# Kernel optimization log

Hardware: AMD Instinct MI355X
Metric: run time of the kernel (lower is better)

Reference implementation:

```python
import jax, jax.numpy as jnp
import numpy as np

B, N, L, D = 16, 8192, 512, 384  # batch, points, latents, model dim
FF = 4 * D  # feedforward inner dim (after GEGLU split)


def _ln(x, g, b, eps=1e-5):
    m = jnp.mean(x, axis=-1, keepdims=True)
    v = jnp.mean((x - m) ** 2, axis=-1, keepdims=True)
    return (x - m) * jax.lax.rsqrt(v + eps) * g + b


def setup_inputs() -> dict:
    key = jax.random.key(0)
    ks = jax.random.split(key, 16)
    s = 0.02
    def w(k, shape):
        return jax.random.normal(k, shape, jnp.float32) * s
    return {
        "x": jax.random.normal(ks[0], (B, N, 3), jnp.float32),
        # MLP: in(3)->D, D->D, D->D, D->D with ReLU between (eqx-style depth=3)
        "mlp_w0": w(ks[1], (3, D)), "mlp_b0": jnp.zeros((D,), jnp.float32),
        "mlp_w1": w(ks[2], (D, D)), "mlp_b1": jnp.zeros((D,), jnp.float32),
        "mlp_w2": w(ks[3], (D, D)), "mlp_b2": jnp.zeros((D,), jnp.float32),
        "mlp_w3": w(ks[4], (D, D)), "mlp_b3": jnp.zeros((D,), jnp.float32),
        "query": jax.random.normal(ks[5], (1, L, D), jnp.float32),
        "ln_q_g": jnp.ones((D,), jnp.float32), "ln_q_b": jnp.zeros((D,), jnp.float32),
        "ln_ctx_g": jnp.ones((D,), jnp.float32), "ln_ctx_b": jnp.zeros((D,), jnp.float32),
        "wq": w(ks[6], (D, D)),
        "wkv": w(ks[7], (D, 2 * D)),
        "wo": w(ks[8], (D, D)), "bo": jnp.zeros((D,), jnp.float32),
        "ln_ff_g": jnp.ones((D,), jnp.float32), "ln_ff_b": jnp.zeros((D,), jnp.float32),
        "ff_w1": w(ks[9], (D, 2 * FF)), "ff_b1": jnp.zeros((2 * FF,), jnp.float32),
        "ff_w2": w(ks[10], (FF, D)), "ff_b2": jnp.zeros((D,), jnp.float32),
    }


def reference(x, mlp_w0, mlp_b0, mlp_w1, mlp_b1, mlp_w2, mlp_b2, mlp_w3, mlp_b3,
              query, ln_q_g, ln_q_b, ln_ctx_g, ln_ctx_b, wq, wkv, wo, bo,
              ln_ff_g, ln_ff_b, ff_w1, ff_b1, ff_w2, ff_b2):
    # point MLP: 3 -> D
    h = jax.nn.relu(x @ mlp_w0 + mlp_b0)
    h = jax.nn.relu(h @ mlp_w1 + mlp_b1)
    h = jax.nn.relu(h @ mlp_w2 + mlp_b2)
    ctx = h @ mlp_w3 + mlp_b3                      # [B, N, D]

    lq = jnp.broadcast_to(query, (x.shape[0], L, D))  # learnable latents

    # PreNorm cross-attention (heads=1, dim_head=D)
    qn = _ln(lq, ln_q_g, ln_q_b)
    cn = _ln(ctx, ln_ctx_g, ln_ctx_b)
    q = qn @ wq                                    # [B, L, D]
    kv = cn @ wkv
    k, v = jnp.split(kv, 2, axis=-1)               # [B, N, D] each
    scale = D ** -0.5
    sim = jnp.einsum('bid,bjd->bij', q, k) * scale # [B, L, N]
    attn = jax.nn.softmax(sim, axis=-1)
    out = jnp.einsum('bij,bjd->bid', attn, v)      # [B, L, D]
    x1 = (out @ wo + bo) + lq                      # residual

    # PreNorm GEGLU feedforward
    f = _ln(x1, ln_ff_g, ln_ff_b)
    f = f @ ff_w1 + ff_b1                          # [B, L, 2*FF]
    a, g = jnp.split(f, 2, axis=-1)
    f = a * jax.nn.gelu(g, approximate=False)      # GEGLU (exact gelu, torch default)
    return (f @ ff_w2 + ff_b2) + x1                # [B, L, D]
```

## Files before the change

### kernel.cpp

```cpp
#include <hip/hip_runtime.h>
#include <math.h>


typedef unsigned short u16;
typedef unsigned int   u32;
typedef __bf16 bf16_t;
typedef bf16_t bf16x8 __attribute__((ext_vector_type(8)));
typedef float  floatx4 __attribute__((ext_vector_type(4)));

__device__ __forceinline__ float b2f(u16 v) {
    return __uint_as_float(((u32)v) << 16);
}
__device__ __forceinline__ u16 f2b(float f) {
    u32 u = __float_as_uint(f);
    return (u16)((u + 0x7FFFu + ((u >> 16) & 1u)) >> 16);
}
__device__ __forceinline__ void stb4(u16* p, float4 f) {
    uint2 v;
    v.x = (u32)f2b(f.x) | ((u32)f2b(f.y) << 16);
    v.y = (u32)f2b(f.z) | ((u32)f2b(f.w) << 16);
    *(uint2*)p = v;
}

__device__ __forceinline__ void gl2lds16(u16* lds, const u16* g) {
    __builtin_amdgcn_global_load_lds(
        (const __attribute__((address_space(1))) void*)g,
        (__attribute__((address_space(3))) void*)lds, 16, 0, 0);
}

__device__ __forceinline__ void xcd_remap(int& bx, int& by, int& bz) {
    int gx = gridDim.x, gy = gridDim.y, gz = gridDim.z;
    int nb = gx * gy * gz;
    int p = bx + gx * (by + gy * bz);
    if ((nb & 7) == 0) {
        int chunk = nb >> 3;
        p = (p & 7) * chunk + (p >> 3);
    }
    bx = p % gx;
    int t = p / gx;
    by = t % gy;
    bz = t / gy;
}

__device__ __forceinline__ void xcd_remap_yf(int& bx, int& by, int& bz) {
    int gx = gridDim.x, gy = gridDim.y, gz = gridDim.z;
    int nb = gx * gy * gz;
    int p = by + gy * (bx + gx * bz);
    if ((nb & 7) == 0) {
        int chunk = nb >> 3;
        p = (p & 7) * chunk + (p >> 3);
    }
    by = p % gy;
    int t = p / gy;
    bx = t % gx;
    bz = t / gx;
}

__global__ __launch_bounds__(256) void wconv_kernel(
    const float* __restrict__ W, u16* __restrict__ WT, int Kd, int Nd)
{
    int idx = blockIdx.x * 256 + threadIdx.x;
    if (idx >= Kd * Nd) return;
    int n = idx / Kd, k = idx - n * Kd;
    WT[idx] = f2b(W[(long long)k * Nd + n]);
}

__global__ __launch_bounds__(256) void layer0_kernel(
    const float* __restrict__ X, const float* __restrict__ W0,
    const float* __restrict__ B0, u16* __restrict__ H, int total4)
{
    int idx = blockIdx.x * 256 + threadIdx.x;
    if (idx >= total4) return;
    int e = idx * 4;
    int m = e / 384;
    int j = e - m * 384;
    float x0 = X[m * 3 + 0], x1 = X[m * 3 + 1], x2 = X[m * 3 + 2];
    float4 w0 = *(const float4*)(W0 + j);
    float4 w1 = *(const float4*)(W0 + 384 + j);
    float4 w2 = *(const float4*)(W0 + 768 + j);
    float4 bb = *(const float4*)(B0 + j);
    float4 v;
    v.x = fmaxf(bb.x + x0 * w0.x + x1 * w1.x + x2 * w2.x, 0.f);
    v.y = fmaxf(bb.y + x0 * w0.y + x1 * w1.y + x2 * w2.y, 0.f);
    v.z = fmaxf(bb.z + x0 * w0.z + x1 * w1.z + x2 * w2.z, 0.f);
    v.w = fmaxf(bb.w + x0 * w0.w + x1 * w1.w + x2 * w2.w, 0.f);
    stb4(H + e, v);
}

template<int IN_F32>
__global__ __launch_bounds__(256) void ln_kernel(
    const void* __restrict__ Xv, const float* __restrict__ g,
    const float* __restrict__ b, u16* __restrict__ Y, int rows)
{
    int w = threadIdx.x >> 6, lane = threadIdx.x & 63;
    int row = blockIdx.x * 4 + w;
    if (row >= rows) return;
    float v[6];
    float s = 0.f, ss = 0.f;
#pragma unroll
    for (int i = 0; i < 6; ++i) {
        int c = i * 64 + lane;
        v[i] = IN_F32 ? ((const float*)Xv)[(long long)row * 384 + c]
                      : b2f(((const u16*)Xv)[(long long)row * 384 + c]);
        s += v[i]; ss += v[i] * v[i];
    }
#pragma unroll
    for (int m = 32; m; m >>= 1) {
        s  += __shfl_xor(s, m, 64);
        ss += __shfl_xor(ss, m, 64);
    }
    float mean = s * (1.0f / 384.0f);
    float var  = ss * (1.0f / 384.0f) - mean * mean;
    float rs = rsqrtf(fmaxf(var, 0.f) + 1e-5f);
    u16* yr = Y + (long long)row * 384;
#pragma unroll
    for (int i = 0; i < 6; ++i) {
        int c = i * 64 + lane;
        yr[c] = f2b((v[i] - mean) * rs * g[c] + b[c]);
    }
}

#define STAGE_AB(bufi, kk)                                                     \
    { u16* asd_ = shmem + (bufi) * 4096;                                       \
      u16* bsd_ = shmem + 8192 + (bufi) * 4096;                                \
      gl2lds16(asd_ + (wv * 32) * 32,                                          \
          aptr_ + (long long)(m0 + wv * 32 + rlo_) * lda_ + (kk) + c8_);       \
      gl2lds16(asd_ + (wv * 32 + 16) * 32,                                     \
          aptr_ + (long long)(m0 + wv * 32 + 16 + rlo_) * lda_ + (kk) + c8_);  \
      gl2lds16(bsd_ + (wv * 32) * 32,                                          \
          bptr_ + (long long)(n0 + wv * 32 + rlo_) * ldb_ + (kk) + c8_);       \
      gl2lds16(bsd_ + (wv * 32 + 16) * 32,                                     \
          bptr_ + (long long)(n0 + wv * 32 + 16 + rlo_) * ldb_ + (kk) + c8_); }

#define MFMA_TILE_DBUF(Aptr, Bptr, LDA, LDB, K0, K1)                           \
    {                                                                          \
        const u16* aptr_ = (Aptr); const u16* bptr_ = (Bptr);                  \
        const long long lda_ = (LDA), ldb_ = (LDB);                            \
        const int rlo_ = lane >> 2, c8_ = (lane & 3) * 8;                      \
        int cur = 0;                                                           \
        STAGE_AB(0, (K0))                                                      \
        for (int k0 = (K0); k0 < (K1); k0 += 32) {                             \
            __syncthreads();           \
            if (k0 + 32 < (K1)) STAGE_AB(cur ^ 1, k0 + 32)                     \
            const u16* As_ = shmem + cur * 4096;                               \
            const u16* Bs_ = shmem + 8192 + cur * 4096;                        \
            bf16x8 a0 = *(const bf16x8*)&As_[(wv * 32 + lr) * 32 + lq * 8];    \
            bf16x8 a1 = *(const bf16x8*)&As_[(wv * 32 + 16 + lr) * 32 + lq * 8]; \
            _Pragma("unroll")                                                  \
            for (int ns = 0; ns < 8; ++ns) {                                   \
                bf16x8 b = *(const bf16x8*)&Bs_[(ns * 16 + lr) * 32 + lq * 8]; \
                acc[0][ns] = __builtin_amdgcn_mfma_f32_16x16x32_bf16(a0, b, acc[0][ns], 0, 0, 0); \
                acc[1][ns] = __builtin_amdgcn_mfma_f32_16x16x32_bf16(a1, b, acc[1][ns], 0, 0, 0); \
            }                                                                  \
            cur ^= 1;                                                          \
        }                                                                      \
    }

template<int RES_F32, int OUT_F32>
__global__ __launch_bounds__(256) void gemm_mfma(
    const u16* __restrict__ A, const u16* __restrict__ WT,
    const float* __restrict__ bias, const void* __restrict__ res,
    void* __restrict__ C,
    int M, int N, int K, int lda, int ldb, int ldc, int ldres,
    float scale, int relu, int resmask,
    long long zsA, long long zsB, long long zsC)
{
    __shared__ u16 shmem[16384];
    const int tid = threadIdx.x;
    const int wv = tid >> 6, lane = tid & 63;
    const int lr = lane & 15, lq = lane >> 4;
    int bx = blockIdx.x, by = blockIdx.y, bz = blockIdx.z;
    xcd_remap_yf(bx, by, bz);
    const int m0 = bx * 128;
    const int n0 = by * 128;
    const u16* Az = A + bz * zsA;
    const u16* Bz = WT + bz * zsB;
    const long long czoff = bz * zsC;

    floatx4 acc[2][8];
#pragma unroll
    for (int i = 0; i < 2; ++i)
#pragma unroll
        for (int j = 0; j < 8; ++j)
            acc[i][j] = (floatx4){0.f, 0.f, 0.f, 0.f};

    MFMA_TILE_DBUF(Az, Bz, lda, ldb, 0, K)

    float bi[8];
#pragma unroll
    for (int ns = 0; ns < 8; ++ns)
        bi[ns] = bias ? bias[n0 + ns * 16 + lr] : 0.f;

#pragma unroll
    for (int ms = 0; ms < 2; ++ms) {
#pragma unroll
        for (int r = 0; r < 4; ++r) {
            int m = m0 + wv * 32 + ms * 16 + lq * 4 + r;
#pragma unroll
            for (int ns = 0; ns < 8; ++ns) {
                int col = n0 + ns * 16 + lr;
                float v = acc[ms][ns][r] * scale + bi[ns];
                if (relu) v = fmaxf(v, 0.f);
                if (res) {
                    long long ro = (long long)(m & resmask) * ldres + col;
                    v += RES_F32 ? ((const float*)res)[ro]
                                 : b2f(((const u16*)res)[ro]);
                }
                long long co = czoff + (long long)m * ldc + col;
                if (OUT_F32) ((float*)C)[co] = v;
                else         ((u16*)C)[co] = f2b(v);
            }
        }
    }
}

__global__ __launch_bounds__(256) void gemm_exp(
    const u16* __restrict__ A, const u16* __restrict__ WT,
    u16* __restrict__ P, float* __restrict__ den,
    int K, int lda, int ldb, int ldc, float scale,
    long long zsB, long long zsP)
{
    __shared__ u16 shmem[16384];
    const int tid = threadIdx.x;
    const int wv = tid >> 6, lane = tid & 63;
    const int lr = lane & 15, lq = lane >> 4;
    int bx = blockIdx.x, by = blockIdx.y, bz = blockIdx.z;
    xcd_remap(bx, by, bz);
    const int m0 = bx * 128;
    const int n0 = by * 128;
    const u16* Bz = WT + bz * zsB;
    u16* Pz = P + bz * zsP;
    float* dz = den + bz * 512;

    floatx4 acc[2][8];
#pragma unroll
    for (int i = 0; i < 2; ++i)
#pragma unroll
        for (int j = 0; j < 8; ++j)
            acc[i][j] = (floatx4){0.f, 0.f, 0.f, 0.f};

    MFMA_TILE_DBUF(A, Bz, lda, ldb, 0, K)

    u16* sh = shmem;
    float srow[2][4] = {};
#pragma unroll
    for (int ms = 0; ms < 2; ++ms) {
        __syncthreads();
#pragma unroll
        for (int ns = 0; ns < 8; ++ns)
#pragma unroll
            for (int r = 0; r < 4; ++r) {
                float l = acc[ms][ns][r] * scale;
                l = fminf(fmaxf(l, -60.f), 60.f);
                float p = __expf(l);
                srow[ms][r] += p;
                sh[(wv * 16 + lq * 4 + r) * 128 + ns * 16 + lr] = f2b(p);
            }
        __syncthreads();
#pragma unroll
        for (int j = 0; j < 4; ++j) {
            int idx = j * 256 + tid;
            int rl = idx >> 4, ch = idx & 15;
            int m = m0 + ((rl >> 4) << 5) + ms * 16 + (rl & 15);
            *(uint4*)&Pz[(long long)m * ldc + n0 + ch * 8] =
                *(const uint4*)&sh[rl * 128 + ch * 8];
        }
    }
#pragma unroll
    for (int ms = 0; ms < 2; ++ms)
#pragma unroll
        for (int r = 0; r < 4; ++r) {
            float s = srow[ms][r];
            s += __shfl_xor(s, 1, 64);
            s += __shfl_xor(s, 2, 64);
            s += __shfl_xor(s, 4, 64);
            s += __shfl_xor(s, 8, 64);
            if (lr == 0)
                atomicAdd(&dz[m0 + wv * 32 + ms * 16 + lq * 4 + r], s);
        }
}

__global__ __launch_bounds__(256) void gemm_pv(
    const u16* __restrict__ P, const u16* __restrict__ VT,
    const float* __restrict__ den, u16* __restrict__ part, int SPLIT)
{
    __shared__ u16 shmem[16384];
    const int tid = threadIdx.x;
    const int wv = tid >> 6, lane = tid & 63;
    const int lr = lane & 15, lq = lane >> 4;
    int bx = blockIdx.x, by = blockIdx.y, bz = blockIdx.z;
    xcd_remap(bx, by, bz);
    const int m0 = bx * 128;
    const int n0 = by * 128;
    const int g = bz / SPLIT, sp = bz - g * SPLIT;
    const int chunk = 8192 / SPLIT;
    const u16* Az = P + (long long)g * 512 * 8192;
    const u16* Bz = VT + (long long)g * 384 * 8192;
    const float* dg = den + g * 512;

    floatx4 acc[2][8];
#pragma unroll
    for (int i = 0; i < 2; ++i)
#pragma unroll
        for (int j = 0; j < 8; ++j)
            acc[i][j] = (floatx4){0.f, 0.f, 0.f, 0.f};

    MFMA_TILE_DBUF(Az, Bz, 8192, 8192, sp * chunk, sp * chunk + chunk)

    u16* pz = part + (long long)bz * 512 * 384;
#pragma unroll
    for (int ms = 0; ms < 2; ++ms)
#pragma unroll
        for (int r = 0; r < 4; ++r) {
            int m = m0 + wv * 32 + ms * 16 + lq * 4 + r;
            float inv = 1.0f / dg[m];
#pragma unroll
            for (int ns = 0; ns < 8; ++ns) {
                int col = n0 + ns * 16 + lr;
                pz[(long long)m * 384 + col] = f2b(acc[ms][ns][r] * inv);
            }
        }
}

__global__ __launch_bounds__(256) void pv_reduce_kernel(
    const u16* __restrict__ part, u16* __restrict__ AO, int SPLIT)
{
    int idx = blockIdx.x * 256 + threadIdx.x;
    int q = idx / 96, j = (idx - q * 96) * 4;
    int g = q >> 9, ql = q & 511;
    const u16* base = part + ((long long)g * SPLIT * 512 + ql) * 384 + j;
    float4 s = make_float4(0.f, 0.f, 0.f, 0.f);
    for (int sp = 0; sp < SPLIT; ++sp) {
        uint2 v = *(const uint2*)(base + (long long)sp * 512 * 384);
        s.x += b2f((u16)(v.x & 0xffff));
        s.y += b2f((u16)(v.x >> 16));
        s.z += b2f((u16)(v.y & 0xffff));
        s.w += b2f((u16)(v.y >> 16));
    }
    stb4(AO + (long long)q * 384 + j, s);
}

__global__ __launch_bounds__(256) void gemm_ff1_geglu(
    const u16* __restrict__ A, const u16* __restrict__ WT,
    const float* __restrict__ bias, u16* __restrict__ C,
    int K, int lda, int ldb, int ldc)
{
    __shared__ u16 shmem[16384];
    const int tid = threadIdx.x;
    const int wv = tid >> 6, lane = tid & 63;
    const int lr = lane & 15, lq = lane >> 4;
    int bx = blockIdx.x, by = blockIdx.y, bz = blockIdx.z;
    xcd_remap_yf(bx, by, bz);
    const int m0 = bx * 128;
    const int n0 = by * 64;
    const int rlo = lane >> 2, c8 = (lane & 3) * 8;

    floatx4 accA[2][4], accG[2][4];
#pragma unroll
    for (int i = 0; i < 2; ++i)
#pragma unroll
        for (int j = 0; j < 4; ++j) {
            accA[i][j] = (floatx4){0.f, 0.f, 0.f, 0.f};
            accG[i][j] = (floatx4){0.f, 0.f, 0.f, 0.f};
        }

#define STAGE_FF(bufi, kk)                                                     \
    { u16* asd = shmem + (bufi) * 4096;                                        \
      u16* bsd = shmem + 8192 + (bufi) * 4096;                                 \
      gl2lds16(asd + (wv * 32) * 32,                                           \
          A + (long long)(m0 + wv * 32 + rlo) * lda + (kk) + c8);              \
      gl2lds16(asd + (wv * 32 + 16) * 32,                                      \
          A + (long long)(m0 + wv * 32 + 16 + rlo) * lda + (kk) + c8);         \
      int r0 = wv * 32 + rlo, r1 = r0 + 16;                                    \
      int wrow0 = (r0 < 64) ? (n0 + r0) : (1536 + n0 + r0 - 64);               \
      int wrow1 = (r1 < 64) ? (n0 + r1) : (1536 + n0 + r1 - 64);               \
      gl2lds16(bsd + (wv * 32) * 32, WT + (long long)wrow0 * ldb + (kk) + c8); \
      gl2lds16(bsd + (wv * 32 + 16) * 32, WT + (long long)wrow1 * ldb + (kk) + c8); }

    int cur = 0;
    STAGE_FF(0, 0)
    for (int k0 = 0; k0 < K; k0 += 32) {
        __syncthreads();
        if (k0 + 32 < K) STAGE_FF(cur ^ 1, k0 + 32)
        const u16* As_ = shmem + cur * 4096;
        const u16* Bs_ = shmem + 8192 + cur * 4096;
        bf16x8 a0 = *(const bf16x8*)&As_[(wv * 32 + lr) * 32 + lq * 8];
        bf16x8 a1 = *(const bf16x8*)&As_[(wv * 32 + 16 + lr) * 32 + lq * 8];
#pragma unroll
        for (int ns = 0; ns < 4; ++ns) {
            bf16x8 bA = *(const bf16x8*)&Bs_[(ns * 16 + lr) * 32 + lq * 8];
            bf16x8 bG = *(const bf16x8*)&Bs_[((64 + ns * 16) + lr) * 32 + lq * 8];
            accA[0][ns] = __builtin_amdgcn_mfma_f32_16x16x32_bf16(a0, bA, accA[0][ns], 0, 0, 0);
            accA[1][ns] = __builtin_amdgcn_mfma_f32_16x16x32_bf16(a1, bA, accA[1][ns], 0, 0, 0);
            accG[0][ns] = __builtin_amdgcn_mfma_f32_16x16x32_bf16(a0, bG, accG[0][ns], 0, 0, 0);
            accG[1][ns] = __builtin_amdgcn_mfma_f32_16x16x32_bf16(a1, bG, accG[1][ns], 0, 0, 0);
        }
        cur ^= 1;
    }
#undef STAGE_FF

    float ba[4], bg[4];
#pragma unroll
    for (int ns = 0; ns < 4; ++ns) {
        ba[ns] = bias[n0 + ns * 16 + lr];
        bg[ns] = bias[1536 + n0 + ns * 16 + lr];
    }
#pragma unroll
    for (int ms = 0; ms < 2; ++ms)
#pragma unroll
        for (int r = 0; r < 4; ++r) {
            int m = m0 + wv * 32 + ms * 16 + lq * 4 + r;
#pragma unroll
            for (int ns = 0; ns < 4; ++ns) {
                int col = n0 + ns * 16 + lr;
                float a = accA[ms][ns][r] + ba[ns];
                float g = accG[ms][ns][r] + bg[ns];
                float v = a * 0.5f * g * (1.0f + erff(g * 0.70710678118654752f));
                C[(long long)m * ldc + col] = f2b(v);
            }
        }
}

extern "C" void kernel_launch(void* const* d_in, const int* in_sizes, int n_in,
                              void* d_out, int out_size, void* d_ws, size_t ws_size,
                              hipStream_t stream) {
    const float* x     = (const float*)d_in[0];
    const float* w0    = (const float*)d_in[1];
    const float* b0    = (const float*)d_in[2];
    const float* w1    = (const float*)d_in[3];
    const float* b1    = (const float*)d_in[4];
    const float* w2    = (const float*)d_in[5];
    const float* b2    = (const float*)d_in[6];
    const float* w3    = (const float*)d_in[7];
    const float* b3    = (const float*)d_in[8];
    const float* query = (const float*)d_in[9];
    const float* lnqg  = (const float*)d_in[10];
    const float* lnqb  = (const float*)d_in[11];
    const float* lncg  = (const float*)d_in[12];
    const float* lncb  = (const float*)d_in[13];
    const float* wq    = (const float*)d_in[14];
    const float* wkv   = (const float*)d_in[15];
    const float* wo    = (const float*)d_in[16];
    const float* bo    = (const float*)d_in[17];
    const float* lnfg  = (const float*)d_in[18];
    const float* lnfb  = (const float*)d_in[19];
    const float* ffw1  = (const float*)d_in[20];
    const float* ffb1  = (const float*)d_in[21];
    const float* ffw2  = (const float*)d_in[22];
    const float* ffb2  = (const float*)d_in[23];
    float* out = (float*)d_out;
    char* wsb = (char*)d_ws;

    auto need = [](int G) -> size_t {
        return (size_t)G * (3LL * 6291456 + 8388608)
             + 25165824
             + 6291456
             + 2 * 393216 + 32768
             + 5603328;
    };
    int G = 2;
    if      (ws_size >= need(16)) G = 16;
    else if (ws_size >= need(8))  G = 8;
    else if (ws_size >= need(4))  G = 4;
    const int SPLIT = 64 / G;

    long long off = 0;
    u16*   bufA   = (u16*)(wsb + off); off += (long long)G * 6291456;
    u16*   bufB   = (u16*)(wsb + off); off += (long long)G * 6291456;
    u16*   VTb    = (u16*)(wsb + off); off += (long long)G * 6291456;
    u16*   Pb     = (u16*)(wsb + off); off += (long long)G * 8388608;
    u16*   part   = (u16*)(wsb + off); off += 25165824;
    u16*   ao_all = (u16*)(wsb + off); off += 6291456;
    u16*   qn     = (u16*)(wsb + off); off += 393216;
    u16*   qb     = (u16*)(wsb + off); off += 393216;
    float* den    = (float*)(wsb + off); off += 32768;
    u16*   w1T    = (u16*)(wsb + off); off += 294912;
    u16*   w2T    = (u16*)(wsb + off); off += 294912;
    u16*   w3T    = (u16*)(wsb + off); off += 294912;
    u16*   wqT    = (u16*)(wsb + off); off += 294912;
    u16*   wkvT   = (u16*)(wsb + off); off += 589824;
    u16*   woT    = (u16*)(wsb + off); off += 294912;
    u16*   ffw1T  = (u16*)(wsb + off); off += 2359296;
    u16*   ffw2T  = (u16*)(wsb + off); off += 1179648;
    u16*   x1_all = (u16*)(wsb + 0);
    u16*   f0_all = (u16*)(wsb + 6291456);
    u16*   gl_all = (u16*)(wsb + 12582912);

    const int FULLMASK = 0x3FFFFFFF;

    wconv_kernel<<<576,  256, 0, stream>>>(w1,   w1T,   384, 384);
    wconv_kernel<<<576,  256, 0, stream>>>(w2,   w2T,   384, 384);
    wconv_kernel<<<576,  256, 0, stream>>>(w3,   w3T,   384, 384);
    wconv_kernel<<<576,  256, 0, stream>>>(wq,   wqT,   384, 384);
    wconv_kernel<<<1152, 256, 0, stream>>>(wkv,  wkvT,  384, 768);
    wconv_kernel<<<576,  256, 0, stream>>>(wo,   woT,   384, 384);
    wconv_kernel<<<4608, 256, 0, stream>>>(ffw1, ffw1T, 384, 3072);
    wconv_kernel<<<2304, 256, 0, stream>>>(ffw2, ffw2T, 1536, 384);
    hipMemsetAsync(den, 0, 16 * 512 * sizeof(float), stream);
    ln_kernel<1><<<128, 256, 0, stream>>>(query, lnqg, lnqb, qn, 512);
    gemm_mfma<0, 0><<<dim3(4, 3), 256, 0, stream>>>(qn, wqT, nullptr, nullptr, qb,
        512, 384, 384, 384, 384, 384, 0, 1.f, 0, FULLMASK, 0, 0, 0);

    const int MG = G * 8192;
    for (int base = 0; base < 16; base += G) {
        const float* xg = x + (long long)base * 24576;

        layer0_kernel<<<G * 3072, 256, 0, stream>>>(xg, w0, b0, bufA, G * 786432);
        gemm_mfma<0, 0><<<dim3(MG / 128, 3), 256, 0, stream>>>(bufA, w1T, b1, nullptr, bufB,
            MG, 384, 384, 384, 384, 384, 0, 1.f, 1, FULLMASK, 0, 0, 0);
        gemm_mfma<0, 0><<<dim3(MG / 128, 3), 256, 0, stream>>>(bufB, w2T, b2, nullptr, bufA,
            MG, 384, 384, 384, 384, 384, 0, 1.f, 1, FULLMASK, 0, 0, 0);
        gemm_mfma<0, 0><<<dim3(MG / 128, 3), 256, 0, stream>>>(bufA, w3T, b3, nullptr, bufB,
            MG, 384, 384, 384, 384, 384, 0, 1.f, 0, FULLMASK, 0, 0, 0);
        ln_kernel<0><<<MG / 4, 256, 0, stream>>>(bufB, lncg, lncb, bufA, MG);
        gemm_mfma<0, 0><<<dim3(MG / 128, 3), 256, 0, stream>>>(bufA, wkvT, nullptr, nullptr, bufB,
            MG, 384, 384, 384, 384, 384, 0, 1.f, 0, FULLMASK, 0, 0, 0);
        gemm_mfma<0, 0><<<dim3(3, 64, G), 256, 0, stream>>>(wkvT + 147456, bufA,
            nullptr, nullptr, VTb, 384, 8192, 384, 384, 384, 8192, 0, 1.f, 0, FULLMASK,
            0, 8192LL * 384, 384LL * 8192);
        gemm_exp<<<dim3(4, 64, G), 256, 0, stream>>>(qb, bufB, Pb, den + base * 512,
            384, 384, 384, 8192, 0.05103103630798288f, 8192LL * 384, 512LL * 8192);
        gemm_pv<<<dim3(4, 3, G * SPLIT), 256, 0, stream>>>(Pb, VTb, den + base * 512,
            part, SPLIT);
        pv_reduce_kernel<<<G * 192, 256, 0, stream>>>(part,
            ao_all + (long long)base * 196608, SPLIT);
    }

    gemm_mfma<1, 0><<<dim3(64, 3), 256, 0, stream>>>(ao_all, woT, bo, query, x1_all,
        8192, 384, 384, 384, 384, 384, 384, 1.f, 0, 511, 0, 0, 0);
    ln_kernel<0><<<2048, 256, 0, stream>>>(x1_all, lnfg, lnfb, f0_all, 8192);
    gemm_ff1_geglu<<<dim3(64, 24), 256, 0, stream>>>(f0_all, ffw1T, ffb1, gl_all,
        384, 384, 384, 1536);
    gemm_mfma<0, 1><<<dim3(64, 3), 256, 0, stream>>>(gl_all, ffw2T, ffb2, x1_all, out,
        8192, 384, 1536, 1536, 1536, 384, 384, 1.f, 0, FULLMASK, 0, 0, 0);
}
```

Before: 881.2 us.

## Switch MFMA GEMM loops to three-stage LDS pipeline with vmcnt waits

Replaces the double-buffered K loop in all MFMA GEMM kernels with a triple-buffered pipeline. Loads are issued two tiles ahead, and each iteration waits only with s_waitcnt vmcnt(4) plus a raw s_barrier instead of a full __syncthreads. The goal is to hide global-to-LDS load latency behind more MFMA work. In exchange, LDS per block grows from 32KB to 48KB, which can reduce occupancy. The design also relies on exact vmcnt accounting, since each stage issues 4 loads per thread.

```diff
diff --git a/kernel.cpp b/kernel.cpp
--- a/kernel.cpp
+++ b/kernel.cpp
@@ -120,9 +120,9 @@
     }
 }
 
-#define STAGE_AB(bufi, kk)                                                     \
+#define STAGE_AB3(bufi, kk)                                                    \
     { u16* asd_ = shmem + (bufi) * 4096;                                       \
-      u16* bsd_ = shmem + 8192 + (bufi) * 4096;                                \
+      u16* bsd_ = shmem + 12288 + (bufi) * 4096;                               \
       gl2lds16(asd_ + (wv * 32) * 32,                                          \
           aptr_ + (long long)(m0 + wv * 32 + rlo_) * lda_ + (kk) + c8_);       \
       gl2lds16(asd_ + (wv * 32 + 16) * 32,                                     \
@@ -132,18 +132,25 @@
       gl2lds16(bsd_ + (wv * 32 + 16) * 32,                                     \
           bptr_ + (long long)(n0 + wv * 32 + 16 + rlo_) * ldb_ + (kk) + c8_); }
 
-#define MFMA_TILE_DBUF(Aptr, Bptr, LDA, LDB, K0, K1)                           \
+#define MFMA_TILE_PIPE(Aptr, Bptr, LDA, LDB, K0, K1)                           \
     {                                                                          \
         const u16* aptr_ = (Aptr); const u16* bptr_ = (Bptr);                  \
         const long long lda_ = (LDA), ldb_ = (LDB);                            \
         const int rlo_ = lane >> 2, c8_ = (lane & 3) * 8;                      \
+        const int T_ = ((K1) - (K0)) >> 5;                                     \
+        STAGE_AB3(0, (K0))                                                     \
+        STAGE_AB3(1, (K0) + 32)                                                \
         int cur = 0;                                                           \
-        STAGE_AB(0, (K0))                                                      \
-        for (int k0 = (K0); k0 < (K1); k0 += 32) {                             \
-            __syncthreads();           \
-            if (k0 + 32 < (K1)) STAGE_AB(cur ^ 1, k0 + 32)                     \
+        for (int t = 0; t < T_; ++t) {                                         \
+            if (t + 1 < T_) { asm volatile("s_waitcnt vmcnt(4)" ::: "memory"); } \
+            else            { asm volatile("s_waitcnt vmcnt(0)" ::: "memory"); } \
+            __builtin_amdgcn_s_barrier();                                      \
+            if (t + 2 < T_) {                                                  \
+                int stg = (cur == 0) ? 2 : cur - 1;                            \
+                STAGE_AB3(stg, (K0) + (t + 2) * 32)                            \
+            }                                                                  \
             const u16* As_ = shmem + cur * 4096;                               \
-            const u16* Bs_ = shmem + 8192 + cur * 4096;                        \
+            const u16* Bs_ = shmem + 12288 + cur * 4096;                       \
             bf16x8 a0 = *(const bf16x8*)&As_[(wv * 32 + lr) * 32 + lq * 8];    \
             bf16x8 a1 = *(const bf16x8*)&As_[(wv * 32 + 16 + lr) * 32 + lq * 8]; \
             _Pragma("unroll")                                                  \
@@ -152,7 +159,7 @@
                 acc[0][ns] = __builtin_amdgcn_mfma_f32_16x16x32_bf16(a0, b, acc[0][ns], 0, 0, 0); \
                 acc[1][ns] = __builtin_amdgcn_mfma_f32_16x16x32_bf16(a1, b, acc[1][ns], 0, 0, 0); \
             }                                                                  \
-            cur ^= 1;                                                          \
+            cur = (cur == 2) ? 0 : cur + 1;                                    \
         }                                                                      \
     }
 
@@ -165,7 +172,7 @@
     float scale, int relu, int resmask,
     long long zsA, long long zsB, long long zsC)
 {
-    __shared__ u16 shmem[16384];
+    __shared__ u16 shmem[24576];
     const int tid = threadIdx.x;
     const int wv = tid >> 6, lane = tid & 63;
     const int lr = lane & 15, lq = lane >> 4;
@@ -184,7 +191,7 @@
         for (int j = 0; j < 8; ++j)
             acc[i][j] = (floatx4){0.f, 0.f, 0.f, 0.f};
 
-    MFMA_TILE_DBUF(Az, Bz, lda, ldb, 0, K)
+    MFMA_TILE_PIPE(Az, Bz, lda, ldb, 0, K)
 
     float bi[8];
 #pragma unroll
@@ -220,7 +227,7 @@
     int K, int lda, int ldb, int ldc, float scale,
     long long zsB, long long zsP)
 {
-    __shared__ u16 shmem[16384];
+    __shared__ u16 shmem[24576];
     const int tid = threadIdx.x;
     const int wv = tid >> 6, lane = tid & 63;
     const int lr = lane & 15, lq = lane >> 4;
@@ -239,7 +246,7 @@
         for (int j = 0; j < 8; ++j)
             acc[i][j] = (floatx4){0.f, 0.f, 0.f, 0.f};
 
-    MFMA_TILE_DBUF(A, Bz, lda, ldb, 0, K)
+    MFMA_TILE_PIPE(A, Bz, lda, ldb, 0, K)
 
     u16* sh = shmem;
     float srow[2][4] = {};
@@ -284,7 +291,7 @@
     const u16* __restrict__ P, const u16* __restrict__ VT,
     const float* __restrict__ den, u16* __restrict__ part, int SPLIT)
 {
-    __shared__ u16 shmem[16384];
+    __shared__ u16 shmem[24576];
     const int tid = threadIdx.x;
     const int wv = tid >> 6, lane = tid & 63;
     const int lr = lane & 15, lq = lane >> 4;
@@ -305,7 +312,7 @@
         for (int j = 0; j < 8; ++j)
             acc[i][j] = (floatx4){0.f, 0.f, 0.f, 0.f};
 
-    MFMA_TILE_DBUF(Az, Bz, 8192, 8192, sp * chunk, sp * chunk + chunk)
+    MFMA_TILE_PIPE(Az, Bz, 8192, 8192, sp * chunk, sp * chunk + chunk)
 
     u16* pz = part + (long long)bz * 512 * 384;
 #pragma unroll
@@ -345,7 +352,7 @@
     const float* __restrict__ bias, u16* __restrict__ C,
     int K, int lda, int ldb, int ldc)
 {
-    __shared__ u16 shmem[16384];
+    __shared__ u16 shmem[24576];
     const int tid = threadIdx.x;
     const int wv = tid >> 6, lane = tid & 63;
     const int lr = lane & 15, lq = lane >> 4;
@@ -366,7 +373,7 @@
 
 #define STAGE_FF(bufi, kk)                                                     \
     { u16* asd = shmem + (bufi) * 4096;                                        \
-      u16* bsd = shmem + 8192 + (bufi) * 4096;                                 \
+      u16* bsd = shmem + 12288 + (bufi) * 4096;                                \
       gl2lds16(asd + (wv * 32) * 32,                                           \
           A + (long long)(m0 + wv * 32 + rlo) * lda + (kk) + c8);              \
       gl2lds16(asd + (wv * 32 + 16) * 32,                                      \
@@ -377,13 +384,20 @@
       gl2lds16(bsd + (wv * 32) * 32, WT + (long long)wrow0 * ldb + (kk) + c8); \
       gl2lds16(bsd + (wv * 32 + 16) * 32, WT + (long long)wrow1 * ldb + (kk) + c8); }
 
+    const int T = K >> 5;
+    STAGE_FF(0, 0)
+    STAGE_FF(1, 32)
     int cur = 0;
-    STAGE_FF(0, 0)
-    for (int k0 = 0; k0 < K; k0 += 32) {
-        __syncthreads();
-        if (k0 + 32 < K) STAGE_FF(cur ^ 1, k0 + 32)
+    for (int t = 0; t < T; ++t) {
+        if (t + 1 < T) { asm volatile("s_waitcnt vmcnt(4)" ::: "memory"); }
+        else           { asm volatile("s_waitcnt vmcnt(0)" ::: "memory"); }
+        __builtin_amdgcn_s_barrier();
+        if (t + 2 < T) {
+            int stg = (cur == 0) ? 2 : cur - 1;
+            STAGE_FF(stg, (t + 2) * 32)
+        }
         const u16* As_ = shmem + cur * 4096;
-        const u16* Bs_ = shmem + 8192 + cur * 4096;
+        const u16* Bs_ = shmem + 12288 + cur * 4096;
         bf16x8 a0 = *(const bf16x8*)&As_[(wv * 32 + lr) * 32 + lq * 8];
         bf16x8 a1 = *(const bf16x8*)&As_[(wv * 32 + 16 + lr) * 32 + lq * 8];
 #pragma unroll
@@ -395,7 +409,7 @@
             accG[0][ns] = __builtin_amdgcn_mfma_f32_16x16x32_bf16(a0, bG, accG[0][ns], 0, 0, 0);
             accG[1][ns] = __builtin_amdgcn_mfma_f32_16x16x32_bf16(a1, bG, accG[1][ns], 0, 0, 0);
         }
-        cur ^= 1;
+        cur = (cur == 2) ? 0 : cur + 1;
     }
 #undef STAGE_FF
 
```

Result: faster. 856.8 us (-2.8%).
